# Kernel tuning notes

Measured on AMD Instinct MI355X. Metric: run time of the kernel, lower is better.

Reference implementation:

```python
import jax, jax.numpy as jnp
import numpy as np

N_NODES = 100000
N_EDGES = 600000
DIM = 128
LN_EPS = 1e-5


def setup_inputs() -> dict:
    key = jax.random.key(0)
    ks = jax.random.split(key, 12)
    s = 1.0 / np.sqrt(DIM)
    return {
        "h": jax.random.normal(ks[0], (N_NODES, DIM), dtype=jnp.float32),
        "edge_src": jax.random.randint(ks[1], (N_EDGES,), 0, N_NODES, dtype=jnp.int32),
        "edge_dst": jax.random.randint(ks[2], (N_EDGES,), 0, N_NODES, dtype=jnp.int32),
        "W_self": jax.random.uniform(ks[3], (DIM, DIM), jnp.float32, -s, s),
        "b_self": jax.random.uniform(ks[4], (DIM,), jnp.float32, -s, s),
        "W_neigh": jax.random.uniform(ks[5], (DIM, DIM), jnp.float32, -s, s),
        "b_neigh": jax.random.uniform(ks[6], (DIM,), jnp.float32, -s, s),
        "W_gate": jax.random.uniform(ks[7], (DIM, 2 * DIM), jnp.float32, -s, s),
        "b_gate": jax.random.uniform(ks[8], (DIM,), jnp.float32, -s, s),
        "ln_gamma": jnp.ones((DIM,), jnp.float32),
        "ln_beta": jnp.zeros((DIM,), jnp.float32),
    }


def reference(h, edge_src, edge_dst, W_self, b_self, W_neigh, b_neigh, W_gate, b_gate, ln_gamma, ln_beta):
    n = h.shape[0]
    # self transform: [N, D]
    hs = h @ W_self.T + b_self
    # mean over predecessors via segment sum over edges (src -> dst)
    neigh_sum = jax.ops.segment_sum(h[edge_src], edge_dst, num_segments=n)
    counts = jax.ops.segment_sum(jnp.ones((edge_src.shape[0],), h.dtype), edge_dst, num_segments=n)
    has_pred = (counts > 0).astype(h.dtype)[:, None]
    neigh_mean = neigh_sum / jnp.maximum(counts, 1.0)[:, None]
    hn = neigh_mean @ W_neigh.T + b_neigh
    # nodes with no predecessors skip the neighbor term entirely (incl. bias)
    m = hs + has_pred * hn
    gate = jax.nn.sigmoid(jnp.concatenate([h, m], axis=-1) @ W_gate.T + b_gate)
    v = gate * m + (1.0 - gate) * h
    # LayerNorm (biased variance, as torch) + relu
    mu = jnp.mean(v, axis=-1, keepdims=True)
    var = jnp.mean(jnp.square(v - mu), axis=-1, keepdims=True)
    out = (v - mu) * jax.lax.rsqrt(var + LN_EPS) * ln_gamma + ln_beta
    return jax.nn.relu(out)
```

## Files before the change

kernel.cpp:

```cpp
#include <hip/hip_runtime.h>
#include <math.h>

#define N_NODES 100000
#define N_EDGES 600000
#define DIM 128
#define LN_EPS 1e-5f
#define SCAN_NBLK ((N_NODES + 255) / 256)
#define NTILES ((N_NODES + 127) / 128)
#define MG_GRID 512

typedef __bf16 bf16x8 __attribute__((ext_vector_type(8)));
typedef __bf16 bf16x4 __attribute__((ext_vector_type(4)));
typedef float f32x4 __attribute__((ext_vector_type(4)));

__global__ __launch_bounds__(256)
void prep_kernel(const float* __restrict__ h, const int* __restrict__ edst,
                 __bf16* __restrict__ h_bf, int* __restrict__ counts) {
  int i = blockIdx.x * 256 + threadIdx.x;
  {
    const float4 v0 = *reinterpret_cast<const float4*>(h + (size_t)i * 8);
    const float4 v1 = *reinterpret_cast<const float4*>(h + (size_t)i * 8 + 4);
    bf16x8 b;
    b[0] = (__bf16)v0.x; b[1] = (__bf16)v0.y; b[2] = (__bf16)v0.z; b[3] = (__bf16)v0.w;
    b[4] = (__bf16)v1.x; b[5] = (__bf16)v1.y; b[6] = (__bf16)v1.z; b[7] = (__bf16)v1.w;
    *reinterpret_cast<bf16x8*>(h_bf + (size_t)i * 8) = b;
  }
  if (i < N_EDGES) atomicAdd(&counts[edst[i]], 1);
}

__global__ __launch_bounds__(256)
void scan1_kernel(const int* __restrict__ counts, int* __restrict__ block_sums) {
  int i = blockIdx.x * 256 + threadIdx.x;
  int v = (i < N_NODES) ? counts[i] : 0;
#pragma unroll
  for (int off = 1; off < 64; off <<= 1) v += __shfl_xor(v, off);
  __shared__ int ws[4];
  if ((threadIdx.x & 63) == 0) ws[threadIdx.x >> 6] = v;
  __syncthreads();
  if (threadIdx.x == 0) block_sums[blockIdx.x] = ws[0] + ws[1] + ws[2] + ws[3];
}

__global__ __launch_bounds__(256)
void scan3_kernel(const int* __restrict__ counts, const int* __restrict__ block_sums,
                  int* __restrict__ row_off, int* __restrict__ cursor) {
  const int i = blockIdx.x * 256 + threadIdx.x;
  const int t = threadIdx.x;
  const int lane = t & 63, wv = t >> 6;
  __shared__ int wtot[4];
  __shared__ int sbase[4];

  int partial = 0;
  for (int j = t; j < blockIdx.x; j += 256) partial += block_sums[j];
#pragma unroll
  for (int off = 1; off < 64; off <<= 1) partial += __shfl_xor(partial, off);
  if (lane == 0) sbase[wv] = partial;
  __syncthreads();
  const int base = sbase[0] + sbase[1] + sbase[2] + sbase[3];

  int v = (i < N_NODES) ? counts[i] : 0;
  int s = v;
#pragma unroll
  for (int off = 1; off < 64; off <<= 1) {
    int u = __shfl_up(s, off);
    if (lane >= off) s += u;
  }
  if (lane == 63) wtot[wv] = s;
  __syncthreads();
  int wo = 0;
  for (int w = 0; w < wv; ++w) wo += wtot[w];
  int excl = base + wo + (s - v);
  if (i < N_NODES) { row_off[i] = excl; cursor[i] = 0; }
  if (i == 0) row_off[N_NODES] = N_EDGES;
}

__global__ __launch_bounds__(256)
void csr_fill_kernel(const int* __restrict__ esrc, const int* __restrict__ edst,
                     const int* __restrict__ row_off, int* __restrict__ cursor,
                     int* __restrict__ csr_src) {
  int base = (blockIdx.x * 256 + threadIdx.x) * 4;
  if (base >= N_EDGES) return;
  int4 s4 = *reinterpret_cast<const int4*>(esrc + base);
  int4 d4 = *reinterpret_cast<const int4*>(edst + base);
  {
    int pos = atomicAdd(&cursor[d4.x], 1);
    csr_src[row_off[d4.x] + pos] = s4.x;
  }
  {
    int pos = atomicAdd(&cursor[d4.y], 1);
    csr_src[row_off[d4.y] + pos] = s4.y;
  }
  {
    int pos = atomicAdd(&cursor[d4.z], 1);
    csr_src[row_off[d4.z] + pos] = s4.z;
  }
  {
    int pos = atomicAdd(&cursor[d4.w], 1);
    csr_src[row_off[d4.w] + pos] = s4.w;
  }
}

__global__ __launch_bounds__(256)
void gather_kernel(const __bf16* __restrict__ h_bf, const int* __restrict__ csr_src,
                   const int* __restrict__ row_off, __bf16* __restrict__ mean_bf) {
  int node = blockIdx.x * 16 + (threadIdx.x >> 4);
  if (node >= N_NODES) return;
  int t = threadIdx.x & 15;
  int b = row_off[node], e = row_off[node + 1];
  float acc[8];
#pragma unroll
  for (int j = 0; j < 8; ++j) acc[j] = 0.f;
  for (int i = b; i < e; i += 8) {
    int idx[8];
#pragma unroll
    for (int j = 0; j < 8; ++j) idx[j] = (i + j < e) ? csr_src[i + j] : -1;
    bf16x8 v[8];
#pragma unroll
    for (int j = 0; j < 8; ++j) {
      if (idx[j] >= 0)
        v[j] = *reinterpret_cast<const bf16x8*>(h_bf + (size_t)idx[j] * DIM + t * 8);
      else
#pragma unroll
        for (int k = 0; k < 8; ++k) v[j][k] = (__bf16)0.f;
    }
#pragma unroll
    for (int j = 0; j < 8; ++j)
#pragma unroll
      for (int k = 0; k < 8; ++k) acc[k] += (float)v[j][k];
  }
  float inv = (e > b) ? 1.0f / (float)(e - b) : 0.0f;
  bf16x8 mv;
#pragma unroll
  for (int j = 0; j < 8; ++j) mv[j] = (__bf16)(acc[j] * inv);
  *reinterpret_cast<bf16x8*>(mean_bf + (size_t)node * DIM + t * 8) = mv;
}

__global__ __launch_bounds__(512, 1)
void m_kernel(const __bf16* __restrict__ h_bf,
              __bf16* __restrict__ mm_bf,
              const int* __restrict__ counts,
              const float* __restrict__ Wself,
              const float* __restrict__ Wneigh,
              const float* __restrict__ b_self,
              const float* __restrict__ b_neigh) {
  __shared__ __align__(16) char smem[81920];
  char* Wl = smem;
  const int tid = threadIdx.x;

  for (int c = tid; c < 4096; c += 512) {
    int mi = c >> 11;
    int w = c & 2047;
    int row = w >> 4, col8 = w & 15;
    const float* src = (mi == 0 ? Wself : Wneigh) + row * 128 + col8 * 8;
    float4 v0 = *reinterpret_cast<const float4*>(src);
    float4 v1 = *reinterpret_cast<const float4*>(src + 4);
    bf16x8 b;
    b[0] = (__bf16)v0.x; b[1] = (__bf16)v0.y; b[2] = (__bf16)v0.z; b[3] = (__bf16)v0.w;
    b[4] = (__bf16)v1.x; b[5] = (__bf16)v1.y; b[6] = (__bf16)v1.z; b[7] = (__bf16)v1.w;
    int byte = (row * 256 + col8 * 16) ^ ((row & 7) << 4);
    *reinterpret_cast<bf16x8*>(Wl + mi * 32768 + byte) = b;
  }
  __syncthreads();

  const int lane = tid & 63;
  const int wave = tid >> 6;
  const int col = lane & 15;
  const int kb = (lane >> 4) << 3;
  const int rloc = (lane >> 4) << 2;
  char* St = smem + 65536 + wave * 2048;

  for (int tile = blockIdx.x; tile < NTILES; tile += MG_GRID) {
    const int node0 = tile * 128;

    bf16x8 a_h[4], a_m[4];
    {
      int n_a = node0 + wave * 16 + col;
      if (n_a < N_NODES) {
#pragma unroll
        for (int k0 = 0; k0 < 4; ++k0) {
          int koff = k0 * 32 + kb;
          a_h[k0] = *reinterpret_cast<const bf16x8*>(h_bf + (size_t)n_a * DIM + koff);
          a_m[k0] = *reinterpret_cast<const bf16x8*>(mm_bf + (size_t)n_a * DIM + koff);
        }
      } else {
#pragma unroll
        for (int k0 = 0; k0 < 4; ++k0)
#pragma unroll
          for (int j = 0; j < 8; ++j) { a_h[k0][j] = (__bf16)0.f; a_m[k0][j] = (__bf16)0.f; }
      }
    }

    int4 c4 = *reinterpret_cast<const int4*>(counts + node0 + wave * 16 + rloc);
    float hp[4];
    {
      int nb0 = node0 + wave * 16 + rloc;
      hp[0] = (nb0 + 0 < N_NODES && c4.x > 0) ? 1.f : 0.f;
      hp[1] = (nb0 + 1 < N_NODES && c4.y > 0) ? 1.f : 0.f;
      hp[2] = (nb0 + 2 < N_NODES && c4.z > 0) ? 1.f : 0.f;
      hp[3] = (nb0 + 3 < N_NODES && c4.w > 0) ? 1.f : 0.f;
    }

    f32x4 sacc[8], nacc[8];
#pragma unroll
    for (int i = 0; i < 8; ++i) {
      sacc[i] = (f32x4){0.f, 0.f, 0.f, 0.f};
      nacc[i] = (f32x4){0.f, 0.f, 0.f, 0.f};
    }
#pragma unroll
    for (int k0 = 0; k0 < 4; ++k0) {
      int koff2 = (k0 * 32 + kb) * 2;
#pragma unroll
      for (int nb = 0; nb < 8; ++nb) {
        int row = nb * 16 + col;
        int swz = (row * 256 + koff2) ^ ((row & 7) << 4);
        bf16x8 bs = *reinterpret_cast<const bf16x8*>(Wl + swz);
        bf16x8 bn = *reinterpret_cast<const bf16x8*>(Wl + 32768 + swz);
        sacc[nb] = __builtin_amdgcn_mfma_f32_16x16x32_bf16(a_h[k0], bs, sacc[nb], 0, 0, 0);
        nacc[nb] = __builtin_amdgcn_mfma_f32_16x16x32_bf16(a_m[k0], bn, nacc[nb], 0, 0, 0);
      }
    }

    bf16x8 am2[4];
#pragma unroll
    for (int half = 0; half < 2; ++half) {
#pragma unroll
      for (int nbl = 0; nbl < 4; ++nbl) {
        int nb = half * 4 + nbl;
        int d = nb * 16 + col;
        float bs = b_self[d], bn = b_neigh[d];
        int offd = d - half * 64;
#pragma unroll
        for (int r = 0; r < 4; ++r) {
          float mval = sacc[nb][r] + bs + hp[r] * (nacc[nb][r] + bn);
          int rl = rloc + r;
          int byte = (rl * 128 + offd * 2) ^ ((rl & 7) << 4);
          *reinterpret_cast<__bf16*>(St + byte) = (__bf16)mval;
        }
      }
#pragma unroll
      for (int kk = 0; kk < 2; ++kk) {
        int k0 = half * 2 + kk;
        int off = k0 * 32 + kb - half * 64;
        int byte = (col * 128 + off * 2) ^ ((col & 7) << 4);
        am2[k0] = *reinterpret_cast<const bf16x8*>(St + byte);
      }
    }

    {
      int n_a = node0 + wave * 16 + col;
      if (n_a < N_NODES) {
#pragma unroll
        for (int k0 = 0; k0 < 4; ++k0)
          *reinterpret_cast<bf16x8*>(mm_bf + (size_t)n_a * DIM + k0 * 32 + kb) = am2[k0];
      }
    }
  }
}

__global__ __launch_bounds__(512, 1)
void g_kernel(const __bf16* __restrict__ h_bf,
              const __bf16* __restrict__ m_bf,
              const float* __restrict__ Wgate,
              const float* __restrict__ b_gate,
              const float* __restrict__ ln_g,
              const float* __restrict__ ln_b,
              float* __restrict__ out) {
  __shared__ __align__(16) char smem[81920];
  char* Wl = smem;
  const int tid = threadIdx.x;

  for (int c = tid; c < 4096; c += 512) {
    int mi = c >> 11;
    int w = c & 2047;
    int row = w >> 4, col8 = w & 15;
    const float* src = Wgate + row * 256 + mi * 128 + col8 * 8;
    float4 v0 = *reinterpret_cast<const float4*>(src);
    float4 v1 = *reinterpret_cast<const float4*>(src + 4);
    bf16x8 b;
    b[0] = (__bf16)v0.x; b[1] = (__bf16)v0.y; b[2] = (__bf16)v0.z; b[3] = (__bf16)v0.w;
    b[4] = (__bf16)v1.x; b[5] = (__bf16)v1.y; b[6] = (__bf16)v1.z; b[7] = (__bf16)v1.w;
    int byte = (row * 256 + col8 * 16) ^ ((row & 7) << 4);
    *reinterpret_cast<bf16x8*>(Wl + mi * 32768 + byte) = b;
  }
  __syncthreads();

  const int lane = tid & 63;
  const int wave = tid >> 6;
  const int col = lane & 15;
  const int kb = (lane >> 4) << 3;
  const int rloc = (lane >> 4) << 2;
  char* St = smem + 65536 + wave * 2048;

  for (int tile = blockIdx.x; tile < NTILES; tile += MG_GRID) {
    const int node0 = tile * 128;

    bf16x8 a_h[4], a_m[4];
    {
      int n_a = node0 + wave * 16 + col;
      if (n_a < N_NODES) {
#pragma unroll
        for (int k0 = 0; k0 < 4; ++k0) {
          int koff = k0 * 32 + kb;
          a_h[k0] = *reinterpret_cast<const bf16x8*>(h_bf + (size_t)n_a * DIM + koff);
          a_m[k0] = *reinterpret_cast<const bf16x8*>(m_bf + (size_t)n_a * DIM + koff);
        }
      } else {
#pragma unroll
        for (int k0 = 0; k0 < 4; ++k0)
#pragma unroll
          for (int j = 0; j < 8; ++j) { a_h[k0][j] = (__bf16)0.f; a_m[k0][j] = (__bf16)0.f; }
      }
    }

    f32x4 gacc[8];
#pragma unroll
    for (int i = 0; i < 8; ++i) gacc[i] = (f32x4){0.f, 0.f, 0.f, 0.f};
#pragma unroll
    for (int k0 = 0; k0 < 4; ++k0) {
      int koff2 = (k0 * 32 + kb) * 2;
#pragma unroll
      for (int nb = 0; nb < 8; ++nb) {
        int row = nb * 16 + col;
        int swz = (row * 256 + koff2) ^ ((row & 7) << 4);
        bf16x8 bgh = *reinterpret_cast<const bf16x8*>(Wl + swz);
        bf16x8 bgm = *reinterpret_cast<const bf16x8*>(Wl + 32768 + swz);
        gacc[nb] = __builtin_amdgcn_mfma_f32_16x16x32_bf16(a_h[k0], bgh, gacc[nb], 0, 0, 0);
        gacc[nb] = __builtin_amdgcn_mfma_f32_16x16x32_bf16(a_m[k0], bgm, gacc[nb], 0, 0, 0);
      }
    }

    bf16x8 gt[4];
#pragma unroll
    for (int half = 0; half < 2; ++half) {
#pragma unroll
      for (int nbl = 0; nbl < 4; ++nbl) {
        int nb = half * 4 + nbl;
        int offd = nb * 16 + col - half * 64;
#pragma unroll
        for (int r = 0; r < 4; ++r) {
          int rl = rloc + r;
          int byte = (rl * 128 + offd * 2) ^ ((rl & 7) << 4);
          *reinterpret_cast<__bf16*>(St + byte) = (__bf16)gacc[nb][r];
        }
      }
#pragma unroll
      for (int kk = 0; kk < 2; ++kk) {
        int k0 = half * 2 + kk;
        int off = k0 * 32 + kb - half * 64;
        int byte = (col * 128 + off * 2) ^ ((col & 7) << 4);
        gt[k0] = *reinterpret_cast<const bf16x8*>(St + byte);
      }
    }

    float s1 = 0.f, s2 = 0.f;
    float vv[4][8];
#pragma unroll
    for (int k0 = 0; k0 < 4; ++k0) {
      int c0 = k0 * 32 + kb;
      float4 bg0 = *reinterpret_cast<const float4*>(b_gate + c0);
      float4 bg1 = *reinterpret_cast<const float4*>(b_gate + c0 + 4);
      float bgv[8] = {bg0.x, bg0.y, bg0.z, bg0.w, bg1.x, bg1.y, bg1.z, bg1.w};
#pragma unroll
      for (int j = 0; j < 8; ++j) {
        float g = 1.0f / (1.0f + __expf(-((float)gt[k0][j] + bgv[j])));
        float v = g * (float)a_m[k0][j] + (1.0f - g) * (float)a_h[k0][j];
        vv[k0][j] = v;
        s1 += v;
        s2 += v * v;
      }
    }
    s1 += __shfl_xor(s1, 16); s1 += __shfl_xor(s1, 32);
    s2 += __shfl_xor(s2, 16); s2 += __shfl_xor(s2, 32);
    float mu = s1 * (1.0f / DIM);
    float var = s2 * (1.0f / DIM) - mu * mu;
    float rs = rsqrtf(var + LN_EPS);

    {
      int gn = node0 + wave * 16 + col;
      bool valid = gn < N_NODES;
#pragma unroll
      for (int k0 = 0; k0 < 4; ++k0) {
        int c0 = k0 * 32 + kb;
        float4 g0 = *reinterpret_cast<const float4*>(ln_g + c0);
        float4 g1 = *reinterpret_cast<const float4*>(ln_g + c0 + 4);
        float4 e0 = *reinterpret_cast<const float4*>(ln_b + c0);
        float4 e1 = *reinterpret_cast<const float4*>(ln_b + c0 + 4);
        float4 o0, o1;
        o0.x = fmaxf((vv[k0][0] - mu) * rs * g0.x + e0.x, 0.f);
        o0.y = fmaxf((vv[k0][1] - mu) * rs * g0.y + e0.y, 0.f);
        o0.z = fmaxf((vv[k0][2] - mu) * rs * g0.z + e0.z, 0.f);
        o0.w = fmaxf((vv[k0][3] - mu) * rs * g0.w + e0.w, 0.f);
        o1.x = fmaxf((vv[k0][4] - mu) * rs * g1.x + e1.x, 0.f);
        o1.y = fmaxf((vv[k0][5] - mu) * rs * g1.y + e1.y, 0.f);
        o1.z = fmaxf((vv[k0][6] - mu) * rs * g1.z + e1.z, 0.f);
        o1.w = fmaxf((vv[k0][7] - mu) * rs * g1.w + e1.w, 0.f);
        if (valid) {
          *reinterpret_cast<float4*>(out + (size_t)gn * DIM + c0) = o0;
          *reinterpret_cast<float4*>(out + (size_t)gn * DIM + c0 + 4) = o1;
        }
      }
    }
  }
}

extern "C" void kernel_launch(void* const* d_in, const int* in_sizes, int n_in,
                              void* d_out, int out_size, void* d_ws, size_t ws_size,
                              hipStream_t stream) {
  const float* h      = (const float*)d_in[0];
  const int*   esrc   = (const int*)d_in[1];
  const int*   edst   = (const int*)d_in[2];
  const float* Wself  = (const float*)d_in[3];
  const float* bself  = (const float*)d_in[4];
  const float* Wneigh = (const float*)d_in[5];
  const float* bneigh = (const float*)d_in[6];
  const float* Wgate  = (const float*)d_in[7];
  const float* bgate  = (const float*)d_in[8];
  const float* ln_g   = (const float*)d_in[9];
  const float* ln_b   = (const float*)d_in[10];
  float* out = (float*)d_out;

  char* ws = (char*)d_ws;
  int* counts   = (int*)ws;
  int* row_off  = (int*)(ws + 400384);
  int* cursor   = (int*)(ws + 800768);
  int* csr_src  = (int*)(ws + 1200768);
  int* blk_sums = (int*)(ws + 3600768);
  __bf16* h_bf    = (__bf16*)(ws + 3602432);
  __bf16* mm_bf   = (__bf16*)(ws + 29202432);

  hipMemsetAsync(counts, 0, (size_t)N_NODES * sizeof(int), stream);

  prep_kernel<<<6250, 256, 0, stream>>>(h, edst, h_bf, counts);
  scan1_kernel<<<SCAN_NBLK, 256, 0, stream>>>(counts, blk_sums);
  scan3_kernel<<<SCAN_NBLK, 256, 0, stream>>>(counts, blk_sums, row_off, cursor);
  csr_fill_kernel<<<(N_EDGES / 4 + 255) / 256, 256, 0, stream>>>(esrc, edst, row_off, cursor, csr_src);
  gather_kernel<<<(N_NODES + 15) / 16, 256, 0, stream>>>(h_bf, csr_src, row_off, mm_bf);
  m_kernel<<<MG_GRID, 512, 0, stream>>>(h_bf, mm_bf, counts, Wself, Wneigh, bself, bneigh);
  g_kernel<<<MG_GRID, 512, 0, stream>>>(h_bf, mm_bf, Wgate, bgate, ln_g, ln_b, out);
}
```

Measured before the change: 167.2 us.

## Fuse self/neighbor transform and gated LayerNorm into one node kernel

```diff
diff --git a/kernel.cpp b/kernel.cpp
--- a/kernel.cpp
+++ b/kernel.cpp
@@ -6,8 +6,8 @@
 #define DIM 128
 #define LN_EPS 1e-5f
 #define SCAN_NBLK ((N_NODES + 255) / 256)
-#define NTILES ((N_NODES + 127) / 128)
-#define MG_GRID 512
+#define NTILES2 ((N_NODES + 255) / 256)
+#define NODE_GRID 256
 
 typedef __bf16 bf16x8 __attribute__((ext_vector_type(8)));
 typedef __bf16 bf16x4 __attribute__((ext_vector_type(4)));
@@ -134,23 +134,33 @@
   *reinterpret_cast<bf16x8*>(mean_bf + (size_t)node * DIM + t * 8) = mv;
 }
 
-__global__ __launch_bounds__(512, 1)
-void m_kernel(const __bf16* __restrict__ h_bf,
-              __bf16* __restrict__ mm_bf,
-              const int* __restrict__ counts,
-              const float* __restrict__ Wself,
-              const float* __restrict__ Wneigh,
-              const float* __restrict__ b_self,
-              const float* __restrict__ b_neigh) {
-  __shared__ __align__(16) char smem[81920];
+__global__ __launch_bounds__(1024, 1)
+void node_kernel(const __bf16* __restrict__ h_bf,
+                 const __bf16* __restrict__ mean_bf,
+                 const int* __restrict__ counts,
+                 const float* __restrict__ Wself,
+                 const float* __restrict__ Wneigh,
+                 const float* __restrict__ Wgate,
+                 const float* __restrict__ b_self,
+                 const float* __restrict__ b_neigh,
+                 const float* __restrict__ b_gate,
+                 const float* __restrict__ ln_g,
+                 const float* __restrict__ ln_b,
+                 float* __restrict__ out) {
+  __shared__ __align__(16) char smem[163840];
   char* Wl = smem;
+
   const int tid = threadIdx.x;
 
-  for (int c = tid; c < 4096; c += 512) {
+  for (int c = tid; c < 8192; c += 1024) {
     int mi = c >> 11;
     int w = c & 2047;
     int row = w >> 4, col8 = w & 15;
-    const float* src = (mi == 0 ? Wself : Wneigh) + row * 128 + col8 * 8;
+    const float* src;
+    if (mi == 0)      src = Wself  + row * 128 + col8 * 8;
+    else if (mi == 1) src = Wneigh + row * 128 + col8 * 8;
+    else if (mi == 2) src = Wgate  + row * 256 + col8 * 8;
+    else              src = Wgate  + row * 256 + 128 + col8 * 8;
     float4 v0 = *reinterpret_cast<const float4*>(src);
     float4 v1 = *reinterpret_cast<const float4*>(src + 4);
     bf16x8 b;
@@ -166,27 +176,26 @@
   const int col = lane & 15;
   const int kb = (lane >> 4) << 3;
   const int rloc = (lane >> 4) << 2;
-  char* St = smem + 65536 + wave * 2048;
-
-  for (int tile = blockIdx.x; tile < NTILES; tile += MG_GRID) {
-    const int node0 = tile * 128;
+  char* St = smem + 131072 + wave * 2048;
+
+  for (int tile = blockIdx.x; tile < NTILES2; tile += NODE_GRID) {
+    const int node0 = tile * 256;
+    const int n_a = node0 + wave * 16 + col;
+    const bool va = n_a < N_NODES;
 
     bf16x8 a_h[4], a_m[4];
-    {
-      int n_a = node0 + wave * 16 + col;
-      if (n_a < N_NODES) {
-#pragma unroll
-        for (int k0 = 0; k0 < 4; ++k0) {
-          int koff = k0 * 32 + kb;
-          a_h[k0] = *reinterpret_cast<const bf16x8*>(h_bf + (size_t)n_a * DIM + koff);
-          a_m[k0] = *reinterpret_cast<const bf16x8*>(mm_bf + (size_t)n_a * DIM + koff);
-        }
-      } else {
-#pragma unroll
-        for (int k0 = 0; k0 < 4; ++k0)
-#pragma unroll
-          for (int j = 0; j < 8; ++j) { a_h[k0][j] = (__bf16)0.f; a_m[k0][j] = (__bf16)0.f; }
-      }
+    if (va) {
+#pragma unroll
+      for (int k0 = 0; k0 < 4; ++k0) {
+        int koff = k0 * 32 + kb;
+        a_h[k0] = *reinterpret_cast<const bf16x8*>(h_bf + (size_t)n_a * DIM + koff);
+        a_m[k0] = *reinterpret_cast<const bf16x8*>(mean_bf + (size_t)n_a * DIM + koff);
+      }
+    } else {
+#pragma unroll
+      for (int k0 = 0; k0 < 4; ++k0)
+#pragma unroll
+        for (int j = 0; j < 8; ++j) { a_h[k0][j] = (__bf16)0.f; a_m[k0][j] = (__bf16)0.f; }
     }
 
     int4 c4 = *reinterpret_cast<const int4*>(counts + node0 + wave * 16 + rloc);
@@ -245,72 +254,6 @@
       }
     }
 
-    {
-      int n_a = node0 + wave * 16 + col;
-      if (n_a < N_NODES) {
-#pragma unroll
-        for (int k0 = 0; k0 < 4; ++k0)
-          *reinterpret_cast<bf16x8*>(mm_bf + (size_t)n_a * DIM + k0 * 32 + kb) = am2[k0];
-      }
-    }
-  }
-}
-
-__global__ __launch_bounds__(512, 1)
-void g_kernel(const __bf16* __restrict__ h_bf,
-              const __bf16* __restrict__ m_bf,
-              const float* __restrict__ Wgate,
-              const float* __restrict__ b_gate,
-              const float* __restrict__ ln_g,
-              const float* __restrict__ ln_b,
-              float* __restrict__ out) {
-  __shared__ __align__(16) char smem[81920];
-  char* Wl = smem;
-  const int tid = threadIdx.x;
-
-  for (int c = tid; c < 4096; c += 512) {
-    int mi = c >> 11;
-    int w = c & 2047;
-    int row = w >> 4, col8 = w & 15;
-    const float* src = Wgate + row * 256 + mi * 128 + col8 * 8;
-    float4 v0 = *reinterpret_cast<const float4*>(src);
-    float4 v1 = *reinterpret_cast<const float4*>(src + 4);
-    bf16x8 b;
-    b[0] = (__bf16)v0.x; b[1] = (__bf16)v0.y; b[2] = (__bf16)v0.z; b[3] = (__bf16)v0.w;
-    b[4] = (__bf16)v1.x; b[5] = (__bf16)v1.y; b[6] = (__bf16)v1.z; b[7] = (__bf16)v1.w;
-    int byte = (row * 256 + col8 * 16) ^ ((row & 7) << 4);
-    *reinterpret_cast<bf16x8*>(Wl + mi * 32768 + byte) = b;
-  }
-  __syncthreads();
-
-  const int lane = tid & 63;
-  const int wave = tid >> 6;
-  const int col = lane & 15;
-  const int kb = (lane >> 4) << 3;
-  const int rloc = (lane >> 4) << 2;
-  char* St = smem + 65536 + wave * 2048;
-
-  for (int tile = blockIdx.x; tile < NTILES; tile += MG_GRID) {
-    const int node0 = tile * 128;
-
-    bf16x8 a_h[4], a_m[4];
-    {
-      int n_a = node0 + wave * 16 + col;
-      if (n_a < N_NODES) {
-#pragma unroll
-        for (int k0 = 0; k0 < 4; ++k0) {
-          int koff = k0 * 32 + kb;
-          a_h[k0] = *reinterpret_cast<const bf16x8*>(h_bf + (size_t)n_a * DIM + koff);
-          a_m[k0] = *reinterpret_cast<const bf16x8*>(m_bf + (size_t)n_a * DIM + koff);
-        }
-      } else {
-#pragma unroll
-        for (int k0 = 0; k0 < 4; ++k0)
-#pragma unroll
-          for (int j = 0; j < 8; ++j) { a_h[k0][j] = (__bf16)0.f; a_m[k0][j] = (__bf16)0.f; }
-      }
-    }
-
     f32x4 gacc[8];
 #pragma unroll
     for (int i = 0; i < 8; ++i) gacc[i] = (f32x4){0.f, 0.f, 0.f, 0.f};
@@ -321,10 +264,10 @@
       for (int nb = 0; nb < 8; ++nb) {
         int row = nb * 16 + col;
         int swz = (row * 256 + koff2) ^ ((row & 7) << 4);
-        bf16x8 bgh = *reinterpret_cast<const bf16x8*>(Wl + swz);
-        bf16x8 bgm = *reinterpret_cast<const bf16x8*>(Wl + 32768 + swz);
+        bf16x8 bgh = *reinterpret_cast<const bf16x8*>(Wl + 65536 + swz);
+        bf16x8 bgm = *reinterpret_cast<const bf16x8*>(Wl + 98304 + swz);
         gacc[nb] = __builtin_amdgcn_mfma_f32_16x16x32_bf16(a_h[k0], bgh, gacc[nb], 0, 0, 0);
-        gacc[nb] = __builtin_amdgcn_mfma_f32_16x16x32_bf16(a_m[k0], bgm, gacc[nb], 0, 0, 0);
+        gacc[nb] = __builtin_amdgcn_mfma_f32_16x16x32_bf16(am2[k0], bgm, gacc[nb], 0, 0, 0);
       }
     }
 
@@ -362,7 +305,7 @@
 #pragma unroll
       for (int j = 0; j < 8; ++j) {
         float g = 1.0f / (1.0f + __expf(-((float)gt[k0][j] + bgv[j])));
-        float v = g * (float)a_m[k0][j] + (1.0f - g) * (float)a_h[k0][j];
+        float v = g * (float)am2[k0][j] + (1.0f - g) * (float)a_h[k0][j];
         vv[k0][j] = v;
         s1 += v;
         s2 += v * v;
@@ -374,9 +317,7 @@
     float var = s2 * (1.0f / DIM) - mu * mu;
     float rs = rsqrtf(var + LN_EPS);
 
-    {
-      int gn = node0 + wave * 16 + col;
-      bool valid = gn < N_NODES;
+    if (va) {
 #pragma unroll
       for (int k0 = 0; k0 < 4; ++k0) {
         int c0 = k0 * 32 + kb;
@@ -393,10 +334,8 @@
         o1.y = fmaxf((vv[k0][5] - mu) * rs * g1.y + e1.y, 0.f);
         o1.z = fmaxf((vv[k0][6] - mu) * rs * g1.z + e1.z, 0.f);
         o1.w = fmaxf((vv[k0][7] - mu) * rs * g1.w + e1.w, 0.f);
-        if (valid) {
-          *reinterpret_cast<float4*>(out + (size_t)gn * DIM + c0) = o0;
-          *reinterpret_cast<float4*>(out + (size_t)gn * DIM + c0 + 4) = o1;
-        }
+        *reinterpret_cast<float4*>(out + (size_t)n_a * DIM + c0) = o0;
+        *reinterpret_cast<float4*>(out + (size_t)n_a * DIM + c0 + 4) = o1;
       }
     }
   }
@@ -425,7 +364,7 @@
   int* csr_src  = (int*)(ws + 1200768);
   int* blk_sums = (int*)(ws + 3600768);
   __bf16* h_bf    = (__bf16*)(ws + 3602432);
-  __bf16* mm_bf   = (__bf16*)(ws + 29202432);
+  __bf16* mean_bf = (__bf16*)(ws + 29202432);
 
   hipMemsetAsync(counts, 0, (size_t)N_NODES * sizeof(int), stream);
 
@@ -433,7 +372,8 @@
   scan1_kernel<<<SCAN_NBLK, 256, 0, stream>>>(counts, blk_sums);
   scan3_kernel<<<SCAN_NBLK, 256, 0, stream>>>(counts, blk_sums, row_off, cursor);
   csr_fill_kernel<<<(N_EDGES / 4 + 255) / 256, 256, 0, stream>>>(esrc, edst, row_off, cursor, csr_src);
-  gather_kernel<<<(N_NODES + 15) / 16, 256, 0, stream>>>(h_bf, csr_src, row_off, mm_bf);
-  m_kernel<<<MG_GRID, 512, 0, stream>>>(h_bf, mm_bf, counts, Wself, Wneigh, bself, bneigh);
-  g_kernel<<<MG_GRID, 512, 0, stream>>>(h_bf, mm_bf, Wgate, bgate, ln_g, ln_b, out);
-}
+  gather_kernel<<<(N_NODES + 15) / 16, 256, 0, stream>>>(h_bf, csr_src, row_off, mean_bf);
+  node_kernel<<<NODE_GRID, 1024, 0, stream>>>(
+      h_bf, mean_bf, counts, Wself, Wneigh, Wgate,
+      bself, bneigh, bgate, ln_g, ln_b, out);
+}
```

Result: slower. 222.8 us (+33.2%).
